# Performance work log

Measured on AMD Instinct MI355X. Metric: run time of the kernel, lower is better.

The kernel has to match this reference:

```python
import jax, jax.numpy as jnp
import numpy as np

N_ATOMS = 50000
N_EDGES = 1600000
NAB = 128   # n_atom_basis
NRBF = 20   # n_rbf
NF = 128    # n_filters

LOG2 = float(np.log(2.0))

def shifted_softplus(x):
    return jax.nn.softplus(x) - LOG2

def setup_inputs() -> dict:
    key = jax.random.key(0)
    ks = jax.random.split(key, 16)
    x = jax.random.normal(ks[0], (N_ATOMS, NAB), dtype=jnp.float32)
    f_ij = jax.random.normal(ks[1], (N_EDGES, NRBF), dtype=jnp.float32)
    rcut_ij = jax.random.uniform(ks[2], (N_EDGES,), dtype=jnp.float32)
    idx_i = jnp.sort(jax.random.randint(ks[3], (N_EDGES,), 0, N_ATOMS))
    idx_j = jax.random.randint(ks[4], (N_EDGES,), 0, N_ATOMS)
    def xavier(k, shape):
        fan_in, fan_out = shape
        s = float(np.sqrt(6.0 / (fan_in + fan_out)))
        return jax.random.uniform(k, shape, dtype=jnp.float32, minval=-s, maxval=s)
    # in2f: Dense(NAB, NF, bias=False)
    W_in2f = xavier(ks[5], (NAB, NF))
    # filter_network: Dense(NRBF, NF, act=ssp), Dense(NF, NF)
    W_f1 = xavier(ks[6], (NRBF, NF)); b_f1 = jnp.zeros((NF,), jnp.float32)
    W_f2 = xavier(ks[7], (NF, NF));   b_f2 = jnp.zeros((NF,), jnp.float32)
    # f2out: Dense(NF, NAB, act=ssp), Dense(NAB, NAB)
    W_o1 = xavier(ks[8], (NF, NAB));  b_o1 = jnp.zeros((NAB,), jnp.float32)
    W_o2 = xavier(ks[9], (NAB, NAB)); b_o2 = jnp.zeros((NAB,), jnp.float32)
    return {"x": x, "f_ij": f_ij, "rcut_ij": rcut_ij, "idx_i": idx_i, "idx_j": idx_j,
            "W_in2f": W_in2f, "W_f1": W_f1, "b_f1": b_f1, "W_f2": W_f2, "b_f2": b_f2,
            "W_o1": W_o1, "b_o1": b_o1, "W_o2": W_o2, "b_o2": b_o2}

def reference(x, f_ij, rcut_ij, idx_i, idx_j,
              W_in2f, W_f1, b_f1, W_f2, b_f2, W_o1, b_o1, W_o2, b_o2):
    # in2f (no bias, no activation): [N, NF]
    h = x @ W_in2f
    # filter network on radial basis: [E, NF]
    Wij = shifted_softplus(f_ij @ W_f1 + b_f1) @ W_f2 + b_f2
    Wij = Wij * rcut_ij[:, None]
    # cfconv: gather neighbor features, modulate by filter, scatter-sum to centers
    x_ij = h[idx_j] * Wij                      # [E, NF]
    y = jax.ops.segment_sum(x_ij, idx_i, num_segments=N_ATOMS)  # [N, NF]
    # f2out
    out = shifted_softplus(y @ W_o1 + b_o1) @ W_o2 + b_o2       # [N, NAB]
    return out
```

## Files before the change

kernel.cpp:

```cpp
#include <hip/hip_runtime.h>
#include <math.h>

#define N_ATOMS 50000
#define N_EDGES 1600000
#define NRBF 20
#define TILE_E 32
#define N_TILES (N_EDGES / TILE_E)

typedef __attribute__((ext_vector_type(8))) short bf16x8;
typedef __attribute__((ext_vector_type(4))) short s16x4;
typedef __attribute__((ext_vector_type(4))) float f32x4;

__device__ __forceinline__ float sp(float v) {
    const float a = fabsf(v);
    const float e = exp2f(a * -1.4426950408889634f);
    const float l = log2f(1.0f + e);
    return fmaxf(v, 0.0f) + l * 0.6931471805599453f;
}
__device__ __forceinline__ float ssp(float v) {
    return sp(v) - 0.6931471805599453f;
}
__device__ __forceinline__ unsigned short f2bf(float f) {
    unsigned int u = __float_as_uint(f);
    u += 0x7fff + ((u >> 16) & 1);
    return (unsigned short)(u >> 16);
}
__device__ __forceinline__ float bf2f(unsigned short b) {
    return __uint_as_float(((unsigned int)b) << 16);
}
__device__ __forceinline__ void lds_barrier() {
    __asm__ __volatile__("s_waitcnt lgkmcnt(0)\ns_barrier" ::: "memory");
}

template<bool SSP_ACT, bool BIAS>
__global__ __launch_bounds__(512) void rowgemm2(
    const float* __restrict__ A, const float* __restrict__ W,
    const float* __restrict__ bias, float* __restrict__ C, int nrows)
{
    __shared__ short sAh[32][136];
    __shared__ short sAl[32][136];

    const int tid  = threadIdx.x;
    const int wave = tid >> 6, lane = tid & 63;
    const int l15  = lane & 15, quad = lane >> 4;
    const int rhalf = wave >> 2, cpair = wave & 3;
    const int r0 = rhalf * 16;
    const int ntiles = (nrows + 31) >> 5;
    const int stride = gridDim.x;

    const int sr0 = tid >> 5;
    const int sr1 = sr0 + 16;
    const int sc0 = (tid & 31) * 4;

    bf16x8 wh[2][4], wl[2][4];
    float br[2];
    #pragma unroll
    for (int ct = 0; ct < 2; ++ct) {
        const int c = cpair * 32 + ct * 16 + l15;
        br[ct] = BIAS ? bias[c] : 0.0f;
        #pragma unroll
        for (int kk = 0; kk < 4; ++kk) {
            #pragma unroll
            for (int j = 0; j < 8; ++j) {
                const int k = kk * 32 + quad * 8 + j;
                const float v = W[k * 128 + c];
                const unsigned short hb = f2bf(v);
                wh[ct][kk][j] = (short)hb;
                wl[ct][kk][j] = (short)f2bf(v - bf2f(hb));
            }
        }
    }

    int t = blockIdx.x;
    if (t >= ntiles) return;

    float4 v0, v1;
    {
        const int ra = t * 32 + sr0, rb = t * 32 + sr1;
        v0 = *(const float4*)(A + (size_t)((ra < nrows) ? ra : nrows - 1) * 128 + sc0);
        v1 = *(const float4*)(A + (size_t)((rb < nrows) ? rb : nrows - 1) * 128 + sc0);
    }

    while (true) {
        {
            const float fa[4] = {v0.x, v0.y, v0.z, v0.w};
            const float fb[4] = {v1.x, v1.y, v1.z, v1.w};
            s16x4 ha, la, hbv, lb;
            #pragma unroll
            for (int j = 0; j < 4; ++j) {
                const unsigned short h0 = f2bf(fa[j]);
                ha[j] = (short)h0; la[j] = (short)f2bf(fa[j] - bf2f(h0));
                const unsigned short h1 = f2bf(fb[j]);
                hbv[j] = (short)h1; lb[j] = (short)f2bf(fb[j] - bf2f(h1));
            }
            *(s16x4*)(&sAh[sr0][sc0]) = ha;  *(s16x4*)(&sAl[sr0][sc0]) = la;
            *(s16x4*)(&sAh[sr1][sc0]) = hbv; *(s16x4*)(&sAl[sr1][sc0]) = lb;
        }
        __syncthreads();

        const int tn = t + stride;
        const bool more = (tn < ntiles);
        float4 n0, n1;
        if (more) {
            const int ra = tn * 32 + sr0, rb = tn * 32 + sr1;
            n0 = *(const float4*)(A + (size_t)((ra < nrows) ? ra : nrows - 1) * 128 + sc0);
            n1 = *(const float4*)(A + (size_t)((rb < nrows) ? rb : nrows - 1) * 128 + sc0);
        }

        bf16x8 ah[4], al[4];
        #pragma unroll
        for (int kk = 0; kk < 4; ++kk) {
            ah[kk] = *(const bf16x8*)(&sAh[r0 + l15][kk * 32 + quad * 8]);
            al[kk] = *(const bf16x8*)(&sAl[r0 + l15][kk * 32 + quad * 8]);
        }
        #pragma unroll
        for (int ct = 0; ct < 2; ++ct) {
            f32x4 acc = {0.0f, 0.0f, 0.0f, 0.0f};
            #pragma unroll
            for (int kk = 0; kk < 4; ++kk) {
                acc = __builtin_amdgcn_mfma_f32_16x16x32_bf16(ah[kk], wh[ct][kk], acc, 0, 0, 0);
                acc = __builtin_amdgcn_mfma_f32_16x16x32_bf16(al[kk], wh[ct][kk], acc, 0, 0, 0);
                acc = __builtin_amdgcn_mfma_f32_16x16x32_bf16(ah[kk], wl[ct][kk], acc, 0, 0, 0);
            }
            const int c = cpair * 32 + ct * 16 + l15;
            #pragma unroll
            for (int r = 0; r < 4; ++r) {
                const int row = t * 32 + r0 + quad * 4 + r;
                if (row < nrows) {
                    float v = acc[r] + br[ct];
                    if (SSP_ACT) v = ssp(v);
                    C[(size_t)row * 128 + c] = v;
                }
            }
        }
        if (!more) break;
        __syncthreads();
        v0 = n0; v1 = n1; t = tn;
    }
}

__global__ __launch_bounds__(512, 2) void edge_mfma(
    const float* __restrict__ f_ij, const float* __restrict__ rcut,
    const int* __restrict__ idx_i, const int* __restrict__ idx_j,
    const float* __restrict__ h,
    const float* __restrict__ W1, const float* __restrict__ b1,
    const float* __restrict__ W2, const float* __restrict__ b2,
    float* __restrict__ y)
{
    __shared__ unsigned short sTH[32][136];
    __shared__ float sXT[128][33];

    const int tid  = threadIdx.x;
    const int wave = tid >> 6, lane = tid & 63;
    const int l15  = lane & 15, quad = lane >> 4;
    const int rhalf = wave >> 2, cpair = wave & 3;
    const int r0  = rhalf * 16;
    const int c0  = cpair * 32 + l15;
    const int rr  = r0 + quad * 4;
    const int col = tid & 127, qtr = tid >> 7;

    bf16x8 w1h[2];
    bf16x8 w2h[2][4];
    float b1r[2], b2r[2];
    #pragma unroll
    for (int ct = 0; ct < 2; ++ct) {
        const int c = c0 + ct * 16;
        b1r[ct] = b1[c];
        #pragma unroll
        for (int j = 0; j < 8; ++j) {
            const int k = quad * 8 + j;
            w1h[ct][j] = (short)f2bf((k < NRBF) ? W1[k * 128 + c] : 0.0f);
        }
        float csum = 0.0f;
        #pragma unroll
        for (int kk = 0; kk < 4; ++kk) {
            #pragma unroll
            for (int j = 0; j < 8; ++j) {
                const float wv = W2[(kk * 32 + quad * 8 + j) * 128 + c];
                const unsigned short hb = f2bf(wv);
                w2h[ct][kk][j] = (short)hb;
                csum += bf2f(hb);
            }
        }
        csum += __shfl_xor(csum, 16);
        csum += __shfl_xor(csum, 32);
        b2r[ct] = b2[c] - 0.6931471805599453f * csum;
    }

    const int nb = gridDim.x;
    const int t0 = (int)(((long long)blockIdx.x * N_TILES) / nb);
    const int t1 = (int)(((long long)(blockIdx.x + 1) * N_TILES) / nb);
    if (t0 >= t1) return;

    int   curI = idx_i[(size_t)t0 * TILE_E];
    float accV = 0.0f;

    float4 apa, apb;
    float  arc0, arc1, arc2, arc3;
    float  ahn[2][4];
    int    jn0, jn1, jn2v, jn3;

    {
        const int e0 = t0 * TILE_E;
        const float* rp = f_ij + (size_t)(e0 + r0 + l15) * NRBF;
        float4 za = {0,0,0,0}, zb = {0,0,0,0};
        if (quad < 2)       { za = *(const float4*)(rp + quad * 8); zb = *(const float4*)(rp + quad * 8 + 4); }
        else if (quad == 2) { za = *(const float4*)(rp + 16); }
        apa = za; apb = zb;
        const float4 rq = *(const float4*)(rcut + e0 + rr);
        arc0 = rq.x; arc1 = rq.y; arc2 = rq.z; arc3 = rq.w;
        const int4 j0 = *(const int4*)(idx_j + e0 + rr);
        const int o0 = j0.x * 128 + c0, o1 = j0.y * 128 + c0;
        const int o2 = j0.z * 128 + c0, o3 = j0.w * 128 + c0;
        ahn[0][0] = h[o0]; ahn[0][1] = h[o1]; ahn[0][2] = h[o2]; ahn[0][3] = h[o3];
        ahn[1][0] = h[o0 + 16]; ahn[1][1] = h[o1 + 16];
        ahn[1][2] = h[o2 + 16]; ahn[1][3] = h[o3 + 16];
        const int tn = (t0 + 1 < N_TILES) ? t0 + 1 : N_TILES - 1;
        const int4 j1 = *(const int4*)(idx_j + tn * TILE_E + rr);
        jn0 = j1.x * 128 + c0; jn1 = j1.y * 128 + c0;
        jn2v = j1.z * 128 + c0; jn3 = j1.w * 128 + c0;
    }

    for (int t = t0; t < t1; ++t) {
        const int e0 = t * TILE_E;
        const int ta = (t + 1 < N_TILES) ? t + 1 : N_TILES - 1;
        const int tb = (t + 2 < N_TILES) ? t + 2 : N_TILES - 1;

        int ii[8];
        {
            const int4 i0 = *(const int4*)(idx_i + e0 + qtr * 8);
            const int4 i1 = *(const int4*)(idx_i + e0 + qtr * 8 + 4);
            ii[0] = i0.x; ii[1] = i0.y; ii[2] = i0.z; ii[3] = i0.w;
            ii[4] = i1.x; ii[5] = i1.y; ii[6] = i1.z; ii[7] = i1.w;
        }
        float4 npa = {0,0,0,0}, npb = {0,0,0,0};
        {
            const float* rp = f_ij + (size_t)(ta * TILE_E + r0 + l15) * NRBF;
            if (quad < 2)       { npa = *(const float4*)(rp + quad * 8); npb = *(const float4*)(rp + quad * 8 + 4); }
            else if (quad == 2) { npa = *(const float4*)(rp + 16); }
        }
        float nrc0, nrc1, nrc2, nrc3;
        {
            const float4 rq = *(const float4*)(rcut + ta * TILE_E + rr);
            nrc0 = rq.x; nrc1 = rq.y; nrc2 = rq.z; nrc3 = rq.w;
        }
        int j20, j21, j22, j23;
        {
            const int4 jq = *(const int4*)(idx_j + tb * TILE_E + rr);
            j20 = jq.x * 128 + c0; j21 = jq.y * 128 + c0;
            j22 = jq.z * 128 + c0; j23 = jq.w * 128 + c0;
        }
        float nhn[2][4];
        nhn[0][0] = h[jn0]; nhn[0][1] = h[jn1]; nhn[0][2] = h[jn2v]; nhn[0][3] = h[jn3];
        nhn[1][0] = h[jn0 + 16]; nhn[1][1] = h[jn1 + 16];
        nhn[1][2] = h[jn2v + 16]; nhn[1][3] = h[jn3 + 16];

        {
            const float va[8] = {apa.x, apa.y, apa.z, apa.w, apb.x, apb.y, apb.z, apb.w};
            bf16x8 ah, al;
            #pragma unroll
            for (int j = 0; j < 8; ++j) {
                const unsigned short hb = f2bf(va[j]);
                ah[j] = (short)hb;
                al[j] = (short)f2bf(va[j] - bf2f(hb));
            }
            #pragma unroll
            for (int ct = 0; ct < 2; ++ct) {
                f32x4 d = {0.0f, 0.0f, 0.0f, 0.0f};
                d = __builtin_amdgcn_mfma_f32_16x16x32_bf16(ah, w1h[ct], d, 0, 0, 0);
                d = __builtin_amdgcn_mfma_f32_16x16x32_bf16(al, w1h[ct], d, 0, 0, 0);
                const int c = c0 + ct * 16;
                #pragma unroll
                for (int r = 0; r < 4; ++r)
                    sTH[rr + r][c] = f2bf(sp(d[r] + b1r[ct]));
            }
        }
        lds_barrier();

        {
            bf16x8 ath[4];
            #pragma unroll
            for (int kk = 0; kk < 4; ++kk)
                ath[kk] = *(const bf16x8*)(&sTH[r0 + l15][kk * 32 + quad * 8]);
            const float arcv[4] = {arc0, arc1, arc2, arc3};
            #pragma unroll
            for (int ct = 0; ct < 2; ++ct) {
                f32x4 acc = {0.0f, 0.0f, 0.0f, 0.0f};
                #pragma unroll
                for (int kk = 0; kk < 4; ++kk)
                    acc = __builtin_amdgcn_mfma_f32_16x16x32_bf16(ath[kk], w2h[ct][kk], acc, 0, 0, 0);
                const int c = c0 + ct * 16;
                #pragma unroll
                for (int r = 0; r < 4; ++r) {
                    const float wij = (acc[r] + b2r[ct]) * arcv[r];
                    sXT[c][rr + r] = wij * ahn[ct][r];
                }
            }
        }
        lds_barrier();

        #pragma unroll
        for (int r = 0; r < 8; ++r) {
            const float v = sXT[col][qtr * 8 + r];
            const int i = ii[r];
            if (i != curI) {
                atomicAdd(&y[curI * 128 + col], accV);
                curI = i; accV = v;
            } else accV += v;
        }

        apa = npa; apb = npb;
        arc0 = nrc0; arc1 = nrc1; arc2 = nrc2; arc3 = nrc3;
        #pragma unroll
        for (int ct = 0; ct < 2; ++ct)
            #pragma unroll
            for (int r = 0; r < 4; ++r) ahn[ct][r] = nhn[ct][r];
        jn0 = j20; jn1 = j21; jn2v = j22; jn3 = j23;
    }
    atomicAdd(&y[curI * 128 + col], accV);
}

extern "C" void kernel_launch(void* const* d_in, const int* in_sizes, int n_in,
                              void* d_out, int out_size, void* d_ws, size_t ws_size,
                              hipStream_t stream) {
    const float* x      = (const float*)d_in[0];
    const float* f_ij   = (const float*)d_in[1];
    const float* rcut   = (const float*)d_in[2];
    const int*   idx_i  = (const int*)d_in[3];
    const int*   idx_j  = (const int*)d_in[4];
    const float* W_in2f = (const float*)d_in[5];
    const float* W_f1   = (const float*)d_in[6];
    const float* b_f1   = (const float*)d_in[7];
    const float* W_f2   = (const float*)d_in[8];
    const float* b_f2   = (const float*)d_in[9];
    const float* W_o1   = (const float*)d_in[10];
    const float* b_o1   = (const float*)d_in[11];
    const float* W_o2   = (const float*)d_in[12];
    const float* b_o2   = (const float*)d_in[13];

    float* out = (float*)d_out;
    float* h   = (float*)d_ws;

    hipMemsetAsync(out, 0, (size_t)N_ATOMS * 128 * sizeof(float), stream);

    rowgemm2<false, false><<<512, 512, 0, stream>>>(x, W_in2f, nullptr, h, N_ATOMS);
    edge_mfma<<<768, 512, 0, stream>>>(f_ij, rcut, idx_i, idx_j, h,
                                       W_f1, b_f1, W_f2, b_f2, out);
    rowgemm2<true, true><<<512, 512, 0, stream>>>(out, W_o1, b_o1, h, N_ATOMS);
    rowgemm2<false, true><<<512, 512, 0, stream>>>(h, W_o2, b_o2, out, N_ATOMS);
}
```

Measured before the change: 690.2 us.

## Fuse output zeroing, simplify edge prefetch, vectorize LDS and add segment fast path

Zeroing of the output is folded into the first row-GEMM kernel instead of a separate memset. The edge kernel drops its two-tile-deep prefetch of h and rcut and gathers h for the current tile directly, keeping only next-tile f_ij and idx_j prefetch. Launch bounds move to 8 blocks per CU and the grid grows to 1024 blocks, aiming for higher occupancy. sXT is padded to 36 so it can be written and read as float4, and a fast path sums all eight values when a thread's edges share one segment. Less software prefetch risks exposed gather latency if occupancy does not actually rise, and the tighter launch bound may cause register spills.

After: 1.187 ms. 72.0% more time.

```diff
diff --git a/kernel.cpp b/kernel.cpp
--- a/kernel.cpp
+++ b/kernel.cpp
@@ -18,7 +18,10 @@
     return fmaxf(v, 0.0f) + l * 0.6931471805599453f;
 }
 __device__ __forceinline__ float ssp(float v) {
-    return sp(v) - 0.6931471805599453f;
+    const float a = fabsf(v);
+    const float e = exp2f(a * -1.4426950408889634f);
+    const float l = log2f(1.0f + e);
+    return fmaxf(v, 0.0f) + fmaf(l, 0.6931471805599453f, -0.6931471805599453f);
 }
 __device__ __forceinline__ unsigned short f2bf(float f) {
     unsigned int u = __float_as_uint(f);
@@ -35,10 +38,19 @@
 template<bool SSP_ACT, bool BIAS>
 __global__ __launch_bounds__(512) void rowgemm2(
     const float* __restrict__ A, const float* __restrict__ W,
-    const float* __restrict__ bias, float* __restrict__ C, int nrows)
+    const float* __restrict__ bias, float* __restrict__ C, int nrows,
+    float* __restrict__ zbuf)
 {
     __shared__ short sAh[32][136];
     __shared__ short sAl[32][136];
+
+    if (zbuf) {
+        const int n4 = N_ATOMS * 128 / 4;
+        const float4 z = {0.0f, 0.0f, 0.0f, 0.0f};
+        for (int i = blockIdx.x * blockDim.x + threadIdx.x; i < n4;
+             i += gridDim.x * blockDim.x)
+            ((float4*)zbuf)[i] = z;
+    }
 
     const int tid  = threadIdx.x;
     const int wave = tid >> 6, lane = tid & 63;
@@ -139,7 +151,7 @@
     }
 }
 
-__global__ __launch_bounds__(512, 2) void edge_mfma(
+__global__ __launch_bounds__(512, 8) void edge_mfma(
     const float* __restrict__ f_ij, const float* __restrict__ rcut,
     const int* __restrict__ idx_i, const int* __restrict__ idx_j,
     const float* __restrict__ h,
@@ -148,7 +160,7 @@
     float* __restrict__ y)
 {
     __shared__ unsigned short sTH[32][136];
-    __shared__ float sXT[128][33];
+    __shared__ float sXT[128][36];
 
     const int tid  = threadIdx.x;
     const int wave = tid >> 6, lane = tid & 63;
@@ -195,68 +207,45 @@
     int   curI = idx_i[(size_t)t0 * TILE_E];
     float accV = 0.0f;
 
-    float4 apa, apb;
-    float  arc0, arc1, arc2, arc3;
-    float  ahn[2][4];
-    int    jn0, jn1, jn2v, jn3;
-
+    float4 fa, fb;
+    unsigned j0o, j1o, j2o, j3o;
     {
         const int e0 = t0 * TILE_E;
         const float* rp = f_ij + (size_t)(e0 + r0 + l15) * NRBF;
         float4 za = {0,0,0,0}, zb = {0,0,0,0};
         if (quad < 2)       { za = *(const float4*)(rp + quad * 8); zb = *(const float4*)(rp + quad * 8 + 4); }
         else if (quad == 2) { za = *(const float4*)(rp + 16); }
-        apa = za; apb = zb;
-        const float4 rq = *(const float4*)(rcut + e0 + rr);
-        arc0 = rq.x; arc1 = rq.y; arc2 = rq.z; arc3 = rq.w;
-        const int4 j0 = *(const int4*)(idx_j + e0 + rr);
-        const int o0 = j0.x * 128 + c0, o1 = j0.y * 128 + c0;
-        const int o2 = j0.z * 128 + c0, o3 = j0.w * 128 + c0;
-        ahn[0][0] = h[o0]; ahn[0][1] = h[o1]; ahn[0][2] = h[o2]; ahn[0][3] = h[o3];
-        ahn[1][0] = h[o0 + 16]; ahn[1][1] = h[o1 + 16];
-        ahn[1][2] = h[o2 + 16]; ahn[1][3] = h[o3 + 16];
-        const int tn = (t0 + 1 < N_TILES) ? t0 + 1 : N_TILES - 1;
-        const int4 j1 = *(const int4*)(idx_j + tn * TILE_E + rr);
-        jn0 = j1.x * 128 + c0; jn1 = j1.y * 128 + c0;
-        jn2v = j1.z * 128 + c0; jn3 = j1.w * 128 + c0;
+        fa = za; fb = zb;
+        const int4 jq = *(const int4*)(idx_j + e0 + rr);
+        j0o = (unsigned)(jq.x << 7) + c0; j1o = (unsigned)(jq.y << 7) + c0;
+        j2o = (unsigned)(jq.z << 7) + c0; j3o = (unsigned)(jq.w << 7) + c0;
     }
 
     for (int t = t0; t < t1; ++t) {
         const int e0 = t * TILE_E;
         const int ta = (t + 1 < N_TILES) ? t + 1 : N_TILES - 1;
-        const int tb = (t + 2 < N_TILES) ? t + 2 : N_TILES - 1;
-
-        int ii[8];
-        {
-            const int4 i0 = *(const int4*)(idx_i + e0 + qtr * 8);
-            const int4 i1 = *(const int4*)(idx_i + e0 + qtr * 8 + 4);
-            ii[0] = i0.x; ii[1] = i0.y; ii[2] = i0.z; ii[3] = i0.w;
-            ii[4] = i1.x; ii[5] = i1.y; ii[6] = i1.z; ii[7] = i1.w;
-        }
-        float4 npa = {0,0,0,0}, npb = {0,0,0,0};
+
+        float hn[2][4];
+        hn[0][0] = h[j0o]; hn[0][1] = h[j1o]; hn[0][2] = h[j2o]; hn[0][3] = h[j3o];
+        hn[1][0] = h[j0o + 16]; hn[1][1] = h[j1o + 16];
+        hn[1][2] = h[j2o + 16]; hn[1][3] = h[j3o + 16];
+
+        const float4 rc = *(const float4*)(rcut + e0 + rr);
+        unsigned nj0, nj1, nj2, nj3;
+        {
+            const int4 jq = *(const int4*)(idx_j + ta * TILE_E + rr);
+            nj0 = (unsigned)(jq.x << 7) + c0; nj1 = (unsigned)(jq.y << 7) + c0;
+            nj2 = (unsigned)(jq.z << 7) + c0; nj3 = (unsigned)(jq.w << 7) + c0;
+        }
+        float4 na = {0,0,0,0}, nb2 = {0,0,0,0};
         {
             const float* rp = f_ij + (size_t)(ta * TILE_E + r0 + l15) * NRBF;
-            if (quad < 2)       { npa = *(const float4*)(rp + quad * 8); npb = *(const float4*)(rp + quad * 8 + 4); }
-            else if (quad == 2) { npa = *(const float4*)(rp + 16); }
-        }
-        float nrc0, nrc1, nrc2, nrc3;
-        {
-            const float4 rq = *(const float4*)(rcut + ta * TILE_E + rr);
-            nrc0 = rq.x; nrc1 = rq.y; nrc2 = rq.z; nrc3 = rq.w;
-        }
-        int j20, j21, j22, j23;
-        {
-            const int4 jq = *(const int4*)(idx_j + tb * TILE_E + rr);
-            j20 = jq.x * 128 + c0; j21 = jq.y * 128 + c0;
-            j22 = jq.z * 128 + c0; j23 = jq.w * 128 + c0;
-        }
-        float nhn[2][4];
-        nhn[0][0] = h[jn0]; nhn[0][1] = h[jn1]; nhn[0][2] = h[jn2v]; nhn[0][3] = h[jn3];
-        nhn[1][0] = h[jn0 + 16]; nhn[1][1] = h[jn1 + 16];
-        nhn[1][2] = h[jn2v + 16]; nhn[1][3] = h[jn3 + 16];
-
-        {
-            const float va[8] = {apa.x, apa.y, apa.z, apa.w, apb.x, apb.y, apb.z, apb.w};
+            if (quad < 2)       { na = *(const float4*)(rp + quad * 8); nb2 = *(const float4*)(rp + quad * 8 + 4); }
+            else if (quad == 2) { na = *(const float4*)(rp + 16); }
+        }
+
+        {
+            const float va[8] = {fa.x, fa.y, fa.z, fa.w, fb.x, fb.y, fb.z, fb.w};
             bf16x8 ah, al;
             #pragma unroll
             for (int j = 0; j < 8; ++j) {
@@ -277,12 +266,14 @@
         }
         lds_barrier();
 
+        const int4 i0 = *(const int4*)(idx_i + e0 + qtr * 8);
+        const int4 i1 = *(const int4*)(idx_i + e0 + qtr * 8 + 4);
+
         {
             bf16x8 ath[4];
             #pragma unroll
             for (int kk = 0; kk < 4; ++kk)
                 ath[kk] = *(const bf16x8*)(&sTH[r0 + l15][kk * 32 + quad * 8]);
-            const float arcv[4] = {arc0, arc1, arc2, arc3};
             #pragma unroll
             for (int ct = 0; ct < 2; ++ct) {
                 f32x4 acc = {0.0f, 0.0f, 0.0f, 0.0f};
@@ -290,32 +281,36 @@
                 for (int kk = 0; kk < 4; ++kk)
                     acc = __builtin_amdgcn_mfma_f32_16x16x32_bf16(ath[kk], w2h[ct][kk], acc, 0, 0, 0);
                 const int c = c0 + ct * 16;
+                float4 xv;
+                xv.x = (acc[0] + b2r[ct]) * rc.x * hn[ct][0];
+                xv.y = (acc[1] + b2r[ct]) * rc.y * hn[ct][1];
+                xv.z = (acc[2] + b2r[ct]) * rc.z * hn[ct][2];
+                xv.w = (acc[3] + b2r[ct]) * rc.w * hn[ct][3];
+                *(float4*)&sXT[c][rr] = xv;
+            }
+        }
+        lds_barrier();
+
+        {
+            const float4 x0 = *(const float4*)&sXT[col][qtr * 8];
+            const float4 x1 = *(const float4*)&sXT[col][qtr * 8 + 4];
+            if (i0.x == curI && i1.w == i0.x) {
+                accV += ((x0.x + x0.y) + (x0.z + x0.w)) + ((x1.x + x1.y) + (x1.z + x1.w));
+            } else {
+                const float v[8] = {x0.x, x0.y, x0.z, x0.w, x1.x, x1.y, x1.z, x1.w};
+                const int   ia[8] = {i0.x, i0.y, i0.z, i0.w, i1.x, i1.y, i1.z, i1.w};
                 #pragma unroll
-                for (int r = 0; r < 4; ++r) {
-                    const float wij = (acc[r] + b2r[ct]) * arcv[r];
-                    sXT[c][rr + r] = wij * ahn[ct][r];
+                for (int r = 0; r < 8; ++r) {
+                    if (ia[r] != curI) {
+                        atomicAdd(&y[curI * 128 + col], accV);
+                        curI = ia[r]; accV = v[r];
+                    } else accV += v[r];
                 }
             }
         }
-        lds_barrier();
-
-        #pragma unroll
-        for (int r = 0; r < 8; ++r) {
-            const float v = sXT[col][qtr * 8 + r];
-            const int i = ii[r];
-            if (i != curI) {
-                atomicAdd(&y[curI * 128 + col], accV);
-                curI = i; accV = v;
-            } else accV += v;
-        }
-
-        apa = npa; apb = npb;
-        arc0 = nrc0; arc1 = nrc1; arc2 = nrc2; arc3 = nrc3;
-        #pragma unroll
-        for (int ct = 0; ct < 2; ++ct)
-            #pragma unroll
-            for (int r = 0; r < 4; ++r) ahn[ct][r] = nhn[ct][r];
-        jn0 = j20; jn1 = j21; jn2v = j22; jn3 = j23;
+
+        fa = na; fb = nb2;
+        j0o = nj0; j1o = nj1; j2o = nj2; j3o = nj3;
     }
     atomicAdd(&y[curI * 128 + col], accV);
 }
@@ -341,11 +336,9 @@
     float* out = (float*)d_out;
     float* h   = (float*)d_ws;
 
-    hipMemsetAsync(out, 0, (size_t)N_ATOMS * 128 * sizeof(float), stream);
-
-    rowgemm2<false, false><<<512, 512, 0, stream>>>(x, W_in2f, nullptr, h, N_ATOMS);
-    edge_mfma<<<768, 512, 0, stream>>>(f_ij, rcut, idx_i, idx_j, h,
-                                       W_f1, b_f1, W_f2, b_f2, out);
-    rowgemm2<true, true><<<512, 512, 0, stream>>>(out, W_o1, b_o1, h, N_ATOMS);
-    rowgemm2<false, true><<<512, 512, 0, stream>>>(h, W_o2, b_o2, out, N_ATOMS);
-}
+    rowgemm2<false, false><<<512, 512, 0, stream>>>(x, W_in2f, nullptr, h, N_ATOMS, out);
+    edge_mfma<<<1024, 512, 0, stream>>>(f_ij, rcut, idx_i, idx_j, h,
+                                        W_f1, b_f1, W_f2, b_f2, out);
+    rowgemm2<true, true><<<512, 512, 0, stream>>>(out, W_o1, b_o1, h, N_ATOMS, nullptr);
+    rowgemm2<false, true><<<512, 512, 0, stream>>>(h, W_o2, b_o2, out, N_ATOMS, nullptr);
+}
```
